# Kernel tuning notes

Measured on AMD Instinct MI355X. Metric: run time of the kernel, lower is better.

## Reference

```python
import jax, jax.numpy as jnp
import numpy as np


def setup_inputs() -> dict:
    key = jax.random.key(0)
    ks = jax.random.split(key, 6)
    B, T, H, U = 32, 2048, 1024, 1024
    return {
        "query": jax.random.normal(ks[0], (1, B, H), dtype=jnp.float32),
        "values": jax.random.normal(ks[1], (B, T, H), dtype=jnp.float32),
        "W_w": jax.random.normal(ks[2], (U, 2 * H), dtype=jnp.float32) * (1.0 / np.sqrt(2 * H)),
        "W_b": jax.random.normal(ks[3], (U,), dtype=jnp.float32) * 0.02,
        "V_w": jax.random.normal(ks[4], (1, U), dtype=jnp.float32) * (1.0 / np.sqrt(U)),
        "V_b": jax.random.normal(ks[5], (1,), dtype=jnp.float32) * 0.02,
    }


def reference(query, values, W_w, W_b, V_w, V_b):
    # query: [1, B, H] -> [B, H]; values: [B, T, H]
    q = query[0]  # squeeze dim 0
    H = values.shape[-1]
    # Split W over the concat dim instead of materializing cat([values, q_rep]):
    # cat @ W.T == values @ W[:, :H].T + q @ W[:, H:].T  (same math as torch)
    Wv, Wq = W_w[:, :H], W_w[:, H:]
    pre = (jnp.einsum("bth,uh->btu", values, Wv)
           + jnp.einsum("bh,uh->bu", q, Wq)[:, None, :]
           + W_b)  # [B, T, U]
    score = jnp.tanh(pre) @ V_w[0] + V_b[0]  # [B, T]
    attention_weights = jax.nn.softmax(score, axis=1)[..., None]  # [B, T, 1]
    context_vector = jnp.sum(attention_weights * values, axis=1)  # [B, H]
    return (context_vector, attention_weights)
```

## Files before the change

### kernel.cpp

```cpp
#include <hip/hip_runtime.h>
#include <hip/hip_bf16.h>


#define B_DIM 32
#define T_DIM 2048
#define H_DIM 1024
#define U_DIM 1024

typedef __bf16 bf16x8 __attribute__((ext_vector_type(8)));
typedef float f32x4 __attribute__((ext_vector_type(4)));

__device__ __forceinline__ unsigned int f2bf(float f) {
    unsigned int u = __float_as_uint(f);
    return (u + 0x7FFFu + ((u >> 16) & 1u)) >> 16;
}

__device__ __forceinline__ float fast_tanh(float x) {
    x = fminf(9.f, fmaxf(-9.f, x));
    float e = __expf(2.f * x);
    return 1.f - 2.f * __frcp_rn(e + 1.f);
}

__global__ void prep_wv_kernel(const float* __restrict__ W_w,
                               unsigned short* __restrict__ wv) {
    int u = blockIdx.x;
    int tid = threadIdx.x;
    float4 x = reinterpret_cast<const float4*>(W_w + (size_t)u * 2 * H_DIM)[tid];
    uint2 p;
    p.x = f2bf(x.x) | (f2bf(x.y) << 16);
    p.y = f2bf(x.z) | (f2bf(x.w) << 16);
    reinterpret_cast<uint2*>(wv)[(size_t)u * (H_DIM / 4) + tid] = p;
}

__global__ void prep_c_kernel(const float* __restrict__ q,
                              const float* __restrict__ W_w,
                              const float* __restrict__ W_b,
                              float* __restrict__ cvec) {
    __shared__ float4 q_sh[4][H_DIM / 4];
    int bg = blockIdx.y;
    int u0 = blockIdx.x * 64;
    int tid = threadIdx.x;
    int lane = tid & 63, w = tid >> 6;
#pragma unroll
    for (int i = 0; i < 4; i++)
        q_sh[i][tid] = reinterpret_cast<const float4*>(
            q + (size_t)(bg * 4 + i) * H_DIM)[tid];
    __syncthreads();
#pragma unroll
    for (int i = 0; i < 16; i++) {
        int u = u0 + w * 16 + i;
        const float4* wr = reinterpret_cast<const float4*>(W_w + (size_t)u * 2 * H_DIM + H_DIM);
        float s0 = 0.f, s1 = 0.f, s2 = 0.f, s3 = 0.f;
#pragma unroll
        for (int j = 0; j < 4; j++) {
            float4 wv4 = wr[j * 64 + lane];
            float4 qa = q_sh[0][j * 64 + lane];
            float4 qb = q_sh[1][j * 64 + lane];
            float4 qc = q_sh[2][j * 64 + lane];
            float4 qd = q_sh[3][j * 64 + lane];
            s0 += wv4.x * qa.x + wv4.y * qa.y + wv4.z * qa.z + wv4.w * qa.w;
            s1 += wv4.x * qb.x + wv4.y * qb.y + wv4.z * qb.z + wv4.w * qb.w;
            s2 += wv4.x * qc.x + wv4.y * qc.y + wv4.z * qc.z + wv4.w * qc.w;
            s3 += wv4.x * qd.x + wv4.y * qd.y + wv4.z * qd.z + wv4.w * qd.w;
        }
#pragma unroll
        for (int off = 32; off >= 1; off >>= 1) {
            s0 += __shfl_xor(s0, off, 64);
            s1 += __shfl_xor(s1, off, 64);
            s2 += __shfl_xor(s2, off, 64);
            s3 += __shfl_xor(s3, off, 64);
        }
        if (lane == 0) {
            float bb = W_b[u];
            cvec[(size_t)(bg * 4 + 0) * U_DIM + u] = s0 + bb;
            cvec[(size_t)(bg * 4 + 1) * U_DIM + u] = s1 + bb;
            cvec[(size_t)(bg * 4 + 2) * U_DIM + u] = s2 + bb;
            cvec[(size_t)(bg * 4 + 3) * U_DIM + u] = s3 + bb;
        }
    }
}

__global__ __launch_bounds__(512, 2)
void gemm_score_kernel(const float* __restrict__ values,
                       const unsigned short* __restrict__ wv,
                       const float* __restrict__ cvec,
                       const float* __restrict__ Vw,
                       float* __restrict__ score) {
    __shared__ __align__(16) unsigned short a_sh[2][64 * 72];
    __shared__ float sc_sh[64 * 8];

    const int tid = threadIdx.x;
    const int lane = tid & 63;
    const int w = tid >> 6;
    const int col = lane & 15;
    const int quad = lane >> 4;
    const int m0 = blockIdx.x * 64;
    const int b = m0 >> 11;
    const int t0 = m0 & (T_DIM - 1);

    f32x4 acc[4][8];
    const f32x4 zero4 = {0.f, 0.f, 0.f, 0.f};
#pragma unroll
    for (int mt = 0; mt < 4; mt++)
#pragma unroll
        for (int nt = 0; nt < 8; nt++) acc[mt][nt] = zero4;

    const int srow = tid >> 3;
    const int skg = tid & 7;
    const float* aptr = values + (size_t)(m0 + srow) * H_DIM + skg * 8;
    const int sidx = srow * 72 + skg * 8;

    {
        float4 n0 = reinterpret_cast<const float4*>(aptr)[0];
        float4 n1 = reinterpret_cast<const float4*>(aptr)[1];
        uint4 pk;
        pk.x = f2bf(n0.x) | (f2bf(n0.y) << 16);
        pk.y = f2bf(n0.z) | (f2bf(n0.w) << 16);
        pk.z = f2bf(n1.x) | (f2bf(n1.y) << 16);
        pk.w = f2bf(n1.z) | (f2bf(n1.w) << 16);
        *reinterpret_cast<uint4*>(&a_sh[0][sidx]) = pk;
    }
    __syncthreads();

    const unsigned short* bbase = wv + (size_t)(w * 128 + col) * H_DIM + quad * 8;

    for (int ks = 0; ks < 16; ks++) {
        const int cur = ks & 1;

        bf16x8 bf[2][8];
#pragma unroll
        for (int kk = 0; kk < 2; kk++)
#pragma unroll
            for (int nt = 0; nt < 8; nt++)
                bf[kk][nt] = *reinterpret_cast<const bf16x8*>(
                    bbase + (size_t)nt * 16 * H_DIM + ks * 64 + kk * 32);

        __builtin_amdgcn_sched_barrier(0x38F);

        float4 n0, n1;
        if (ks < 15) {
            const float* ap = aptr + (ks + 1) * 64;
            n0 = reinterpret_cast<const float4*>(ap)[0];
            n1 = reinterpret_cast<const float4*>(ap)[1];
        }
        __builtin_amdgcn_sched_barrier(0x387);

#pragma unroll
        for (int kk = 0; kk < 2; kk++) {
            bf16x8 af[4];
#pragma unroll
            for (int mt = 0; mt < 4; mt++)
                af[mt] = *reinterpret_cast<const bf16x8*>(
                    &a_sh[cur][(mt * 16 + col) * 72 + kk * 32 + quad * 8]);
#pragma unroll
            for (int nt = 0; nt < 8; nt++)
#pragma unroll
                for (int mt = 0; mt < 4; mt++)
                    acc[mt][nt] = __builtin_amdgcn_mfma_f32_16x16x32_bf16(
                        af[mt], bf[kk][nt], acc[mt][nt], 0, 0, 0);
        }

        if (ks < 15) {
            uint4 pk;
            pk.x = f2bf(n0.x) | (f2bf(n0.y) << 16);
            pk.y = f2bf(n0.z) | (f2bf(n0.w) << 16);
            pk.z = f2bf(n1.x) | (f2bf(n1.y) << 16);
            pk.w = f2bf(n1.z) | (f2bf(n1.w) << 16);
            *reinterpret_cast<uint4*>(&a_sh[1 - cur][sidx]) = pk;
        }
        __syncthreads();
    }

    float cv[8], vwv[8];
#pragma unroll
    for (int nt = 0; nt < 8; nt++) {
        int n = w * 128 + nt * 16 + col;
        cv[nt] = cvec[(size_t)b * U_DIM + n];
        vwv[nt] = Vw[n];
    }
#pragma unroll
    for (int mt = 0; mt < 4; mt++) {
#pragma unroll
        for (int j = 0; j < 4; j++) {
            float s = 0.f;
#pragma unroll
            for (int nt = 0; nt < 8; nt++)
                s += fast_tanh(acc[mt][nt][j] + cv[nt]) * vwv[nt];
            s += __shfl_xor(s, 1, 64);
            s += __shfl_xor(s, 2, 64);
            s += __shfl_xor(s, 4, 64);
            s += __shfl_xor(s, 8, 64);
            if (col == 0) sc_sh[(mt * 16 + quad * 4 + j) * 8 + w] = s;
        }
    }
    __syncthreads();
    if (tid < 64) {
        float s = 0.f;
#pragma unroll
        for (int ww = 0; ww < 8; ww++) s += sc_sh[tid * 8 + ww];
        score[(size_t)b * T_DIM + t0 + tid] = s;
    }
}

__global__ void softmax_kernel(const float* __restrict__ score,
                               float* __restrict__ aw) {
    int b = blockIdx.x;
    int tid = threadIdx.x;
    int lane = tid & 63, w = tid >> 6;
    __shared__ float redm[4];
    __shared__ float reds[4];
    float loc[8];
    float m = -1e30f;
#pragma unroll
    for (int i = 0; i < 8; i++) {
        loc[i] = score[(size_t)b * T_DIM + tid + i * 256];
        m = fmaxf(m, loc[i]);
    }
#pragma unroll
    for (int off = 32; off >= 1; off >>= 1) m = fmaxf(m, __shfl_xor(m, off, 64));
    if (lane == 0) redm[w] = m;
    __syncthreads();
    m = fmaxf(fmaxf(redm[0], redm[1]), fmaxf(redm[2], redm[3]));
    float sum = 0.f;
#pragma unroll
    for (int i = 0; i < 8; i++) {
        loc[i] = __expf(loc[i] - m);
        sum += loc[i];
    }
#pragma unroll
    for (int off = 32; off >= 1; off >>= 1) sum += __shfl_xor(sum, off, 64);
    if (lane == 0) reds[w] = sum;
    __syncthreads();
    sum = reds[0] + reds[1] + reds[2] + reds[3];
    float inv = 1.0f / sum;
#pragma unroll
    for (int i = 0; i < 8; i++)
        aw[(size_t)b * T_DIM + tid + i * 256] = loc[i] * inv;
}

__global__ void ctx_partial_kernel(const float* __restrict__ values,
                                   const float* __restrict__ aw,
                                   float* __restrict__ partial) {
    int tc = blockIdx.x;
    int b = blockIdx.y;
    int tid = threadIdx.x;
    const float4* v4 = reinterpret_cast<const float4*>(
                           values + ((size_t)b * T_DIM + tc * 128) * H_DIM) + tid;
    const float* a = aw + (size_t)b * T_DIM + tc * 128;
    float4 acc = make_float4(0.f, 0.f, 0.f, 0.f);
#pragma unroll 4
    for (int t = 0; t < 128; t++) {
        float wgt = a[t];
        float4 vv = v4[(size_t)t * (H_DIM / 4)];
        acc.x += wgt * vv.x; acc.y += wgt * vv.y;
        acc.z += wgt * vv.z; acc.w += wgt * vv.w;
    }
    reinterpret_cast<float4*>(partial + ((size_t)b * 16 + tc) * H_DIM)[tid] = acc;
}

__global__ void ctx_combine_kernel(const float* __restrict__ partial,
                                   float* __restrict__ ctx) {
    int idx = blockIdx.x * 256 + threadIdx.x;
    int b = idx >> 10, h = idx & (H_DIM - 1);
    float s = 0.f;
#pragma unroll
    for (int tc = 0; tc < 16; tc++)
        s += partial[((size_t)b * 16 + tc) * H_DIM + h];
    ctx[idx] = s;
}

extern "C" void kernel_launch(void* const* d_in, const int* in_sizes, int n_in,
                              void* d_out, int out_size, void* d_ws, size_t ws_size,
                              hipStream_t stream) {
    const float* query  = (const float*)d_in[0];
    const float* values = (const float*)d_in[1];
    const float* W_w    = (const float*)d_in[2];
    const float* W_b    = (const float*)d_in[3];
    const float* V_w    = (const float*)d_in[4];

    float* out = (float*)d_out;
    char* ws = (char*)d_ws;
    float* cvec            = (float*)(ws);
    unsigned short* wv     = (unsigned short*)(ws + 131072);
    float* score           = (float*)(ws + 131072 + 2097152);
    float* partial         = (float*)(ws + 131072 + 2097152 + 262144);
    float* ctx = out;
    float* aw  = out + B_DIM * H_DIM;

    prep_wv_kernel<<<U_DIM, 256, 0, stream>>>(W_w, wv);
    prep_c_kernel<<<dim3(U_DIM / 64, B_DIM / 4), 256, 0, stream>>>(query, W_w, W_b, cvec);
    gemm_score_kernel<<<(B_DIM * T_DIM) / 64, 512, 0, stream>>>(values, wv, cvec, V_w, score);
    softmax_kernel<<<B_DIM, 256, 0, stream>>>(score, aw);
    ctx_partial_kernel<<<dim3(16, B_DIM), 256, 0, stream>>>(values, aw, partial);
    ctx_combine_kernel<<<128, 256, 0, stream>>>(partial, ctx);
}
```

Measured before the change: 692.1 us.

## Retile score GEMM to 256x256 LDS-staged tiles and fuse softmax with context

The score GEMM moves from 64-row tiles that read W directly from global memory into registers to 256x256 output tiles. Both operands are staged through double-buffered, XOR-swizzled LDS, and blocks are ordered so that neighbours share tiles. Each N-tile writes a partial score, and the combined softmax-context kernel sums the four partials, recomputes the softmax in every block, and accumulates the context with atomics. The context output is zeroed in prep_c. This removes the redundant W traffic and two kernel launches, but adds recomputation of the softmax reduction per block, atomic contention, and a large LDS footprint that may lower occupancy.

```diff
diff --git a/kernel.cpp b/kernel.cpp
--- a/kernel.cpp
+++ b/kernel.cpp
@@ -35,12 +35,14 @@
 __global__ void prep_c_kernel(const float* __restrict__ q,
                               const float* __restrict__ W_w,
                               const float* __restrict__ W_b,
-                              float* __restrict__ cvec) {
+                              float* __restrict__ cvec,
+                              float* __restrict__ ctx) {
     __shared__ float4 q_sh[4][H_DIM / 4];
     int bg = blockIdx.y;
     int u0 = blockIdx.x * 64;
     int tid = threadIdx.x;
     int lane = tid & 63, w = tid >> 6;
+    ctx[(size_t)(blockIdx.y * 16 + blockIdx.x) * 256 + tid] = 0.f;
 #pragma unroll
     for (int i = 0; i < 4; i++)
         q_sh[i][tid] = reinterpret_cast<const float4*>(
@@ -85,136 +87,169 @@
                        const unsigned short* __restrict__ wv,
                        const float* __restrict__ cvec,
                        const float* __restrict__ Vw,
-                       float* __restrict__ score) {
-    __shared__ __align__(16) unsigned short a_sh[2][64 * 72];
-    __shared__ float sc_sh[64 * 8];
+                       float* __restrict__ score_part) {
+    __shared__ __align__(16) unsigned short a_sh[2][256 * 64];
+    __shared__ __align__(16) unsigned short b_sh[2][256 * 64];
 
     const int tid = threadIdx.x;
     const int lane = tid & 63;
     const int w = tid >> 6;
     const int col = lane & 15;
     const int quad = lane >> 4;
-    const int m0 = blockIdx.x * 64;
+    const int wr = w >> 2;
+    const int wc = w & 3;
+
+    const int work = (blockIdx.x & 7) * 128 + (blockIdx.x >> 3);
+    const int mtile = work >> 2;
+    const int ntile = work & 3;
+    const int m0 = mtile * 256;
     const int b = m0 >> 11;
-    const int t0 = m0 & (T_DIM - 1);
-
-    f32x4 acc[4][8];
+
+    f32x4 acc[8][4];
     const f32x4 zero4 = {0.f, 0.f, 0.f, 0.f};
 #pragma unroll
-    for (int mt = 0; mt < 4; mt++)
-#pragma unroll
-        for (int nt = 0; nt < 8; nt++) acc[mt][nt] = zero4;
-
-    const int srow = tid >> 3;
-    const int skg = tid & 7;
-    const float* aptr = values + (size_t)(m0 + srow) * H_DIM + skg * 8;
-    const int sidx = srow * 72 + skg * 8;
+    for (int mt = 0; mt < 8; mt++)
+#pragma unroll
+        for (int nt = 0; nt < 4; nt++) acc[mt][nt] = zero4;
+
+    const float4* v4 = reinterpret_cast<const float4*>(values);
+    const uint4* wv4 = reinterpret_cast<const uint4*>(wv);
+
+    const int arb = tid >> 4;
+    const int ak16 = tid & 15;
+    const int asw = (arb & 7) << 3;
+    const int bn = tid >> 1;
+    const int bkh = tid & 1;
+    const int bsw = (bn & 7) << 3;
 
     {
-        float4 n0 = reinterpret_cast<const float4*>(aptr)[0];
-        float4 n1 = reinterpret_cast<const float4*>(aptr)[1];
-        uint4 pk;
-        pk.x = f2bf(n0.x) | (f2bf(n0.y) << 16);
-        pk.y = f2bf(n0.z) | (f2bf(n0.w) << 16);
-        pk.z = f2bf(n1.x) | (f2bf(n1.y) << 16);
-        pk.w = f2bf(n1.z) | (f2bf(n1.w) << 16);
-        *reinterpret_cast<uint4*>(&a_sh[0][sidx]) = pk;
-    }
-    __syncthreads();
-
-    const unsigned short* bbase = wv + (size_t)(w * 128 + col) * H_DIM + quad * 8;
+        uint4 bstg[4];
+        const uint4* bgl = wv4 + (size_t)(ntile * 256 + bn) * 128 + bkh * 4;
+#pragma unroll
+        for (int j = 0; j < 4; j++) bstg[j] = bgl[j];
+        float4 astg[8];
+        const float4* agl = v4 + (size_t)(m0 + arb) * 256 + ak16;
+#pragma unroll
+        for (int j = 0; j < 8; j++) astg[j] = agl[(size_t)8192 * j];
+#pragma unroll
+        for (int j = 0; j < 4; j++)
+            *reinterpret_cast<uint4*>(&b_sh[0][bn * 64 + ((bkh * 32 + j * 8) ^ bsw)]) = bstg[j];
+#pragma unroll
+        for (int j = 0; j < 8; j++) {
+            uint2 p;
+            p.x = f2bf(astg[j].x) | (f2bf(astg[j].y) << 16);
+            p.y = f2bf(astg[j].z) | (f2bf(astg[j].w) << 16);
+            *reinterpret_cast<uint2*>(&a_sh[0][(arb + 32 * j) * 64 + ((ak16 * 4) ^ asw)]) = p;
+        }
+    }
+    __syncthreads();
+
+    const int swz = (col & 7) << 3;
 
     for (int ks = 0; ks < 16; ks++) {
         const int cur = ks & 1;
 
-        bf16x8 bf[2][8];
-#pragma unroll
-        for (int kk = 0; kk < 2; kk++)
-#pragma unroll
-            for (int nt = 0; nt < 8; nt++)
-                bf[kk][nt] = *reinterpret_cast<const bf16x8*>(
-                    bbase + (size_t)nt * 16 * H_DIM + ks * 64 + kk * 32);
-
+        uint4 bstg[4];
+        float4 astg[8];
+        if (ks < 15) {
+            const uint4* bgl = wv4 + (size_t)(ntile * 256 + bn) * 128 + (ks + 1) * 8 + bkh * 4;
+#pragma unroll
+            for (int j = 0; j < 4; j++) bstg[j] = bgl[j];
+            const float4* agl = v4 + (size_t)(m0 + arb) * 256 + (ks + 1) * 16 + ak16;
+#pragma unroll
+            for (int j = 0; j < 8; j++) astg[j] = agl[(size_t)8192 * j];
+        }
         __builtin_amdgcn_sched_barrier(0x38F);
 
-        float4 n0, n1;
+#pragma unroll
+        for (int kk = 0; kk < 2; kk++) {
+            bf16x8 af[8];
+            bf16x8 bf[4];
+#pragma unroll
+            for (int mt = 0; mt < 8; mt++)
+                af[mt] = *reinterpret_cast<const bf16x8*>(
+                    &a_sh[cur][(wr * 128 + mt * 16 + col) * 64 + ((kk * 32 + quad * 8) ^ swz)]);
+#pragma unroll
+            for (int nt = 0; nt < 4; nt++)
+                bf[nt] = *reinterpret_cast<const bf16x8*>(
+                    &b_sh[cur][(wc * 64 + nt * 16 + col) * 64 + ((kk * 32 + quad * 8) ^ swz)]);
+#pragma unroll
+            for (int nt = 0; nt < 4; nt++)
+#pragma unroll
+                for (int mt = 0; mt < 8; mt++)
+                    acc[mt][nt] = __builtin_amdgcn_mfma_f32_16x16x32_bf16(
+                        af[mt], bf[nt], acc[mt][nt], 0, 0, 0);
+            if (kk == 0 && ks < 15) {
+#pragma unroll
+                for (int j = 0; j < 4; j++)
+                    *reinterpret_cast<uint4*>(
+                        &b_sh[1 - cur][bn * 64 + ((bkh * 32 + j * 8) ^ bsw)]) = bstg[j];
+            }
+        }
+
         if (ks < 15) {
-            const float* ap = aptr + (ks + 1) * 64;
-            n0 = reinterpret_cast<const float4*>(ap)[0];
-            n1 = reinterpret_cast<const float4*>(ap)[1];
-        }
-        __builtin_amdgcn_sched_barrier(0x387);
-
-#pragma unroll
-        for (int kk = 0; kk < 2; kk++) {
-            bf16x8 af[4];
-#pragma unroll
-            for (int mt = 0; mt < 4; mt++)
-                af[mt] = *reinterpret_cast<const bf16x8*>(
-                    &a_sh[cur][(mt * 16 + col) * 72 + kk * 32 + quad * 8]);
-#pragma unroll
-            for (int nt = 0; nt < 8; nt++)
-#pragma unroll
-                for (int mt = 0; mt < 4; mt++)
-                    acc[mt][nt] = __builtin_amdgcn_mfma_f32_16x16x32_bf16(
-                        af[mt], bf[kk][nt], acc[mt][nt], 0, 0, 0);
-        }
-
-        if (ks < 15) {
-            uint4 pk;
-            pk.x = f2bf(n0.x) | (f2bf(n0.y) << 16);
-            pk.y = f2bf(n0.z) | (f2bf(n0.w) << 16);
-            pk.z = f2bf(n1.x) | (f2bf(n1.y) << 16);
-            pk.w = f2bf(n1.z) | (f2bf(n1.w) << 16);
-            *reinterpret_cast<uint4*>(&a_sh[1 - cur][sidx]) = pk;
+#pragma unroll
+            for (int j = 0; j < 8; j++) {
+                uint2 p;
+                p.x = f2bf(astg[j].x) | (f2bf(astg[j].y) << 16);
+                p.y = f2bf(astg[j].z) | (f2bf(astg[j].w) << 16);
+                *reinterpret_cast<uint2*>(
+                    &a_sh[1 - cur][(arb + 32 * j) * 64 + ((ak16 * 4) ^ asw)]) = p;
+            }
         }
         __syncthreads();
     }
 
-    float cv[8], vwv[8];
-#pragma unroll
-    for (int nt = 0; nt < 8; nt++) {
-        int n = w * 128 + nt * 16 + col;
+    float* sc = reinterpret_cast<float*>(a_sh);
+    float cv[4], vwv[4];
+#pragma unroll
+    for (int nt = 0; nt < 4; nt++) {
+        int n = ntile * 256 + wc * 64 + nt * 16 + col;
         cv[nt] = cvec[(size_t)b * U_DIM + n];
         vwv[nt] = Vw[n];
     }
 #pragma unroll
-    for (int mt = 0; mt < 4; mt++) {
+    for (int mt = 0; mt < 8; mt++) {
 #pragma unroll
         for (int j = 0; j < 4; j++) {
             float s = 0.f;
 #pragma unroll
-            for (int nt = 0; nt < 8; nt++)
+            for (int nt = 0; nt < 4; nt++)
                 s += fast_tanh(acc[mt][nt][j] + cv[nt]) * vwv[nt];
             s += __shfl_xor(s, 1, 64);
             s += __shfl_xor(s, 2, 64);
             s += __shfl_xor(s, 4, 64);
             s += __shfl_xor(s, 8, 64);
-            if (col == 0) sc_sh[(mt * 16 + quad * 4 + j) * 8 + w] = s;
-        }
-    }
-    __syncthreads();
-    if (tid < 64) {
-        float s = 0.f;
-#pragma unroll
-        for (int ww = 0; ww < 8; ww++) s += sc_sh[tid * 8 + ww];
-        score[(size_t)b * T_DIM + t0 + tid] = s;
-    }
-}
-
-__global__ void softmax_kernel(const float* __restrict__ score,
-                               float* __restrict__ aw) {
-    int b = blockIdx.x;
+            if (col == 0) sc[(wr * 128 + mt * 16 + quad * 4 + j) * 4 + wc] = s;
+        }
+    }
+    __syncthreads();
+    if (tid < 256) {
+        float s = sc[tid * 4] + sc[tid * 4 + 1] + sc[tid * 4 + 2] + sc[tid * 4 + 3];
+        score_part[(size_t)ntile * (B_DIM * T_DIM) + m0 + tid] = s;
+    }
+}
+
+__global__ void ctx_sm_kernel(const float* __restrict__ values,
+                              const float* __restrict__ score_part,
+                              float* __restrict__ aw,
+                              float* __restrict__ ctx) {
+    int tc = blockIdx.x;
+    int b = blockIdx.y;
     int tid = threadIdx.x;
     int lane = tid & 63, w = tid >> 6;
     __shared__ float redm[4];
     __shared__ float reds[4];
+    __shared__ float aw_sh[128];
+    const float* sp = score_part + (size_t)b * T_DIM;
     float loc[8];
     float m = -1e30f;
 #pragma unroll
     for (int i = 0; i < 8; i++) {
-        loc[i] = score[(size_t)b * T_DIM + tid + i * 256];
-        m = fmaxf(m, loc[i]);
+        int t = tid + i * 256;
+        float s = sp[t] + sp[65536 + t] + sp[131072 + t] + sp[196608 + t];
+        loc[i] = s;
+        m = fmaxf(m, s);
     }
 #pragma unroll
     for (int off = 32; off >= 1; off >>= 1) m = fmaxf(m, __shfl_xor(m, off, 64));
@@ -233,40 +268,29 @@
     __syncthreads();
     sum = reds[0] + reds[1] + reds[2] + reds[3];
     float inv = 1.0f / sum;
-#pragma unroll
-    for (int i = 0; i < 8; i++)
-        aw[(size_t)b * T_DIM + tid + i * 256] = loc[i] * inv;
-}
-
-__global__ void ctx_partial_kernel(const float* __restrict__ values,
-                                   const float* __restrict__ aw,
-                                   float* __restrict__ partial) {
-    int tc = blockIdx.x;
-    int b = blockIdx.y;
-    int tid = threadIdx.x;
+    if (tid < 128) {
+        int t = tc * 128 + tid;
+        float s = sp[t] + sp[65536 + t] + sp[131072 + t] + sp[196608 + t];
+        float av = __expf(s - m) * inv;
+        aw[(size_t)b * T_DIM + t] = av;
+        aw_sh[tid] = av;
+    }
+    __syncthreads();
     const float4* v4 = reinterpret_cast<const float4*>(
                            values + ((size_t)b * T_DIM + tc * 128) * H_DIM) + tid;
-    const float* a = aw + (size_t)b * T_DIM + tc * 128;
-    float4 acc = make_float4(0.f, 0.f, 0.f, 0.f);
+    float4 a = make_float4(0.f, 0.f, 0.f, 0.f);
 #pragma unroll 4
     for (int t = 0; t < 128; t++) {
-        float wgt = a[t];
+        float wgt = aw_sh[t];
         float4 vv = v4[(size_t)t * (H_DIM / 4)];
-        acc.x += wgt * vv.x; acc.y += wgt * vv.y;
-        acc.z += wgt * vv.z; acc.w += wgt * vv.w;
-    }
-    reinterpret_cast<float4*>(partial + ((size_t)b * 16 + tc) * H_DIM)[tid] = acc;
-}
-
-__global__ void ctx_combine_kernel(const float* __restrict__ partial,
-                                   float* __restrict__ ctx) {
-    int idx = blockIdx.x * 256 + threadIdx.x;
-    int b = idx >> 10, h = idx & (H_DIM - 1);
-    float s = 0.f;
-#pragma unroll
-    for (int tc = 0; tc < 16; tc++)
-        s += partial[((size_t)b * 16 + tc) * H_DIM + h];
-    ctx[idx] = s;
+        a.x += wgt * vv.x; a.y += wgt * vv.y;
+        a.z += wgt * vv.z; a.w += wgt * vv.w;
+    }
+    float* cp = ctx + (size_t)b * H_DIM + tid * 4;
+    atomicAdd(cp + 0, a.x);
+    atomicAdd(cp + 1, a.y);
+    atomicAdd(cp + 2, a.z);
+    atomicAdd(cp + 3, a.w);
 }
 
 extern "C" void kernel_launch(void* const* d_in, const int* in_sizes, int n_in,
@@ -282,15 +306,12 @@
     char* ws = (char*)d_ws;
     float* cvec            = (float*)(ws);
     unsigned short* wv     = (unsigned short*)(ws + 131072);
-    float* score           = (float*)(ws + 131072 + 2097152);
-    float* partial         = (float*)(ws + 131072 + 2097152 + 262144);
+    float* score_part      = (float*)(ws + 131072 + 2097152);
     float* ctx = out;
     float* aw  = out + B_DIM * H_DIM;
 
     prep_wv_kernel<<<U_DIM, 256, 0, stream>>>(W_w, wv);
-    prep_c_kernel<<<dim3(U_DIM / 64, B_DIM / 4), 256, 0, stream>>>(query, W_w, W_b, cvec);
-    gemm_score_kernel<<<(B_DIM * T_DIM) / 64, 512, 0, stream>>>(values, wv, cvec, V_w, score);
-    softmax_kernel<<<B_DIM, 256, 0, stream>>>(score, aw);
-    ctx_partial_kernel<<<dim3(16, B_DIM), 256, 0, stream>>>(values, aw, partial);
-    ctx_combine_kernel<<<128, 256, 0, stream>>>(partial, ctx);
-}
+    prep_c_kernel<<<dim3(U_DIM / 64, B_DIM / 4), 256, 0, stream>>>(query, W_w, W_b, cvec, ctx);
+    gemm_score_kernel<<<1024, 512, 0, stream>>>(values, wv, cvec, V_w, score_part);
+    ctx_sm_kernel<<<dim3(16, B_DIM), 256, 0, stream>>>(values, score_part, aw, ctx);
+}
```

After: 770.9 us. 1.11x slower.

## Split GEMM N into two tiles, register-prefetch B, hardware bf16 convert

Applied to the files above, without the earlier changes.

The score GEMM now runs 256-thread blocks that each cover 64 rows by 512 units, so the U dimension is split across two blocks. Each block writes a partial score that the softmax kernel adds back together. The K loop uses 32-wide steps with ping-pong register prefetch of the W fragments, v_cvt_pk_bf16_f32 for conversion, s_setprio around the MFMAs, and a remapped block order. The context reduction uses more chunks and stages the attention weights in LDS. The trade-offs are that values are read and converted twice and the K loop issues twice as many barriers.

```diff
diff --git a/kernel.cpp b/kernel.cpp
--- a/kernel.cpp
+++ b/kernel.cpp
@@ -13,6 +13,12 @@
 __device__ __forceinline__ unsigned int f2bf(float f) {
     unsigned int u = __float_as_uint(f);
     return (u + 0x7FFFu + ((u >> 16) & 1u)) >> 16;
+}
+
+__device__ __forceinline__ unsigned int cvt2(float lo, float hi) {
+    unsigned int r;
+    asm("v_cvt_pk_bf16_f32 %0, %1, %2" : "=v"(r) : "v"(lo), "v"(hi));
+    return r;
 }
 
 __device__ __forceinline__ float fast_tanh(float x) {
@@ -80,23 +86,26 @@
     }
 }
 
-__global__ __launch_bounds__(512, 2)
+__global__ __launch_bounds__(256, 2)
 void gemm_score_kernel(const float* __restrict__ values,
                        const unsigned short* __restrict__ wv,
                        const float* __restrict__ cvec,
                        const float* __restrict__ Vw,
-                       float* __restrict__ score) {
-    __shared__ __align__(16) unsigned short a_sh[2][64 * 72];
-    __shared__ float sc_sh[64 * 8];
+                       float* __restrict__ score_part) {
+    __shared__ __align__(16) unsigned short a_sh[2][64 * 32];
+    __shared__ float sc_sh[64 * 4];
 
     const int tid = threadIdx.x;
     const int lane = tid & 63;
     const int w = tid >> 6;
     const int col = lane & 15;
     const int quad = lane >> 4;
-    const int m0 = blockIdx.x * 64;
+
+    const int work = (blockIdx.x & 7) * 256 + (blockIdx.x >> 3);
+    const int mtile = work >> 1;
+    const int ntile = work & 1;
+    const int m0 = mtile * 64;
     const int b = m0 >> 11;
-    const int t0 = m0 & (T_DIM - 1);
 
     f32x4 acc[4][8];
     const f32x4 zero4 = {0.f, 0.f, 0.f, 0.f};
@@ -105,76 +114,71 @@
 #pragma unroll
         for (int nt = 0; nt < 8; nt++) acc[mt][nt] = zero4;
 
-    const int srow = tid >> 3;
-    const int skg = tid & 7;
-    const float* aptr = values + (size_t)(m0 + srow) * H_DIM + skg * 8;
-    const int sidx = srow * 72 + skg * 8;
-
+    const int arow = tid >> 2;
+    const int akq = tid & 3;
+    const float4* agl = reinterpret_cast<const float4*>(
+                            values + (size_t)(m0 + arow) * H_DIM) + akq * 2;
+    unsigned short* adst0 = &a_sh[0][arow * 32 + akq * 8];
+    unsigned short* adst1 = &a_sh[1][arow * 32 + akq * 8];
+
+    const char* bbase = (const char*)wv +
+        (size_t)(ntile * 512 + w * 128 + col) * 2048 + quad * 16;
+
+    bf16x8 bA[8], bB[8];
     {
-        float4 n0 = reinterpret_cast<const float4*>(aptr)[0];
-        float4 n1 = reinterpret_cast<const float4*>(aptr)[1];
+        float4 f0 = agl[0], f1 = agl[1];
         uint4 pk;
-        pk.x = f2bf(n0.x) | (f2bf(n0.y) << 16);
-        pk.y = f2bf(n0.z) | (f2bf(n0.w) << 16);
-        pk.z = f2bf(n1.x) | (f2bf(n1.y) << 16);
-        pk.w = f2bf(n1.z) | (f2bf(n1.w) << 16);
-        *reinterpret_cast<uint4*>(&a_sh[0][sidx]) = pk;
-    }
-    __syncthreads();
-
-    const unsigned short* bbase = wv + (size_t)(w * 128 + col) * H_DIM + quad * 8;
-
-    for (int ks = 0; ks < 16; ks++) {
-        const int cur = ks & 1;
-
-        bf16x8 bf[2][8];
-#pragma unroll
-        for (int kk = 0; kk < 2; kk++)
-#pragma unroll
-            for (int nt = 0; nt < 8; nt++)
-                bf[kk][nt] = *reinterpret_cast<const bf16x8*>(
-                    bbase + (size_t)nt * 16 * H_DIM + ks * 64 + kk * 32);
-
-        __builtin_amdgcn_sched_barrier(0x38F);
-
-        float4 n0, n1;
-        if (ks < 15) {
-            const float* ap = aptr + (ks + 1) * 64;
-            n0 = reinterpret_cast<const float4*>(ap)[0];
-            n1 = reinterpret_cast<const float4*>(ap)[1];
-        }
-        __builtin_amdgcn_sched_barrier(0x387);
-
-#pragma unroll
-        for (int kk = 0; kk < 2; kk++) {
-            bf16x8 af[4];
-#pragma unroll
-            for (int mt = 0; mt < 4; mt++)
-                af[mt] = *reinterpret_cast<const bf16x8*>(
-                    &a_sh[cur][(mt * 16 + col) * 72 + kk * 32 + quad * 8]);
-#pragma unroll
-            for (int nt = 0; nt < 8; nt++)
-#pragma unroll
-                for (int mt = 0; mt < 4; mt++)
-                    acc[mt][nt] = __builtin_amdgcn_mfma_f32_16x16x32_bf16(
-                        af[mt], bf[kk][nt], acc[mt][nt], 0, 0, 0);
-        }
-
-        if (ks < 15) {
-            uint4 pk;
-            pk.x = f2bf(n0.x) | (f2bf(n0.y) << 16);
-            pk.y = f2bf(n0.z) | (f2bf(n0.w) << 16);
-            pk.z = f2bf(n1.x) | (f2bf(n1.y) << 16);
-            pk.w = f2bf(n1.z) | (f2bf(n1.w) << 16);
-            *reinterpret_cast<uint4*>(&a_sh[1 - cur][sidx]) = pk;
-        }
-        __syncthreads();
-    }
+        pk.x = cvt2(f0.x, f0.y); pk.y = cvt2(f0.z, f0.w);
+        pk.z = cvt2(f1.x, f1.y); pk.w = cvt2(f1.z, f1.w);
+        *reinterpret_cast<uint4*>(adst0) = pk;
+#pragma unroll
+        for (int nt = 0; nt < 8; nt++)
+            bA[nt] = *reinterpret_cast<const bf16x8*>(bbase + (size_t)nt * 32768);
+    }
+    __syncthreads();
+
+#define GSTEP(CUR, KS, BC, BN) do {                                            \
+        float4 f0, f1;                                                         \
+        if ((KS) < 31) {                                                       \
+            f0 = agl[((KS) + 1) * 8];                                          \
+            f1 = agl[((KS) + 1) * 8 + 1];                                      \
+            _Pragma("unroll")                                                  \
+            for (int nt = 0; nt < 8; nt++)                                     \
+                BN[nt] = *reinterpret_cast<const bf16x8*>(                     \
+                    bbase + (size_t)nt * 32768 + ((KS) + 1) * 64);             \
+        }                                                                      \
+        bf16x8 af[4];                                                          \
+        _Pragma("unroll")                                                      \
+        for (int mt = 0; mt < 4; mt++)                                         \
+            af[mt] = *reinterpret_cast<const bf16x8*>(                         \
+                &a_sh[CUR][(mt * 16 + col) * 32 + quad * 8]);                  \
+        __builtin_amdgcn_s_setprio(1);                                         \
+        _Pragma("unroll")                                                      \
+        for (int nt = 0; nt < 8; nt++)                                         \
+            _Pragma("unroll")                                                  \
+            for (int mt = 0; mt < 4; mt++)                                     \
+                acc[mt][nt] = __builtin_amdgcn_mfma_f32_16x16x32_bf16(         \
+                    af[mt], BC[nt], acc[mt][nt], 0, 0, 0);                     \
+        __builtin_amdgcn_s_setprio(0);                                         \
+        if ((KS) < 31) {                                                       \
+            uint4 pk;                                                          \
+            pk.x = cvt2(f0.x, f0.y); pk.y = cvt2(f0.z, f0.w);                  \
+            pk.z = cvt2(f1.x, f1.y); pk.w = cvt2(f1.z, f1.w);                  \
+            *reinterpret_cast<uint4*>((CUR) ? adst0 : adst1) = pk;             \
+        }                                                                      \
+        __syncthreads();                                                       \
+    } while (0)
+
+    for (int k2 = 0; k2 < 16; k2++) {
+        GSTEP(0, 2 * k2, bA, bB);
+        GSTEP(1, 2 * k2 + 1, bB, bA);
+    }
+#undef GSTEP
 
     float cv[8], vwv[8];
 #pragma unroll
     for (int nt = 0; nt < 8; nt++) {
-        int n = w * 128 + nt * 16 + col;
+        int n = ntile * 512 + w * 128 + nt * 16 + col;
         cv[nt] = cvec[(size_t)b * U_DIM + n];
         vwv[nt] = Vw[n];
     }
@@ -190,30 +194,31 @@
             s += __shfl_xor(s, 2, 64);
             s += __shfl_xor(s, 4, 64);
             s += __shfl_xor(s, 8, 64);
-            if (col == 0) sc_sh[(mt * 16 + quad * 4 + j) * 8 + w] = s;
+            if (col == 0) sc_sh[(mt * 16 + quad * 4 + j) * 4 + w] = s;
         }
     }
     __syncthreads();
     if (tid < 64) {
-        float s = 0.f;
-#pragma unroll
-        for (int ww = 0; ww < 8; ww++) s += sc_sh[tid * 8 + ww];
-        score[(size_t)b * T_DIM + t0 + tid] = s;
-    }
-}
-
-__global__ void softmax_kernel(const float* __restrict__ score,
+        float s = sc_sh[tid * 4] + sc_sh[tid * 4 + 1] +
+                  sc_sh[tid * 4 + 2] + sc_sh[tid * 4 + 3];
+        score_part[(size_t)ntile * (B_DIM * T_DIM) + m0 + tid] = s;
+    }
+}
+
+__global__ void softmax_kernel(const float* __restrict__ score_part,
                                float* __restrict__ aw) {
     int b = blockIdx.x;
     int tid = threadIdx.x;
     int lane = tid & 63, w = tid >> 6;
     __shared__ float redm[4];
     __shared__ float reds[4];
+    const float* sp = score_part + (size_t)b * T_DIM;
     float loc[8];
     float m = -1e30f;
 #pragma unroll
     for (int i = 0; i < 8; i++) {
-        loc[i] = score[(size_t)b * T_DIM + tid + i * 256];
+        int t = tid + i * 256;
+        loc[i] = sp[t] + sp[B_DIM * T_DIM + t];
         m = fmaxf(m, loc[i]);
     }
 #pragma unroll
@@ -244,18 +249,20 @@
     int tc = blockIdx.x;
     int b = blockIdx.y;
     int tid = threadIdx.x;
+    __shared__ float aw_sh[64];
+    if (tid < 64) aw_sh[tid] = aw[(size_t)b * T_DIM + tc * 64 + tid];
+    __syncthreads();
     const float4* v4 = reinterpret_cast<const float4*>(
-                           values + ((size_t)b * T_DIM + tc * 128) * H_DIM) + tid;
-    const float* a = aw + (size_t)b * T_DIM + tc * 128;
-    float4 acc = make_float4(0.f, 0.f, 0.f, 0.f);
+                           values + ((size_t)b * T_DIM + tc * 64) * H_DIM) + tid;
+    float4 a = make_float4(0.f, 0.f, 0.f, 0.f);
 #pragma unroll 4
-    for (int t = 0; t < 128; t++) {
-        float wgt = a[t];
+    for (int t = 0; t < 64; t++) {
+        float wgt = aw_sh[t];
         float4 vv = v4[(size_t)t * (H_DIM / 4)];
-        acc.x += wgt * vv.x; acc.y += wgt * vv.y;
-        acc.z += wgt * vv.z; acc.w += wgt * vv.w;
-    }
-    reinterpret_cast<float4*>(partial + ((size_t)b * 16 + tc) * H_DIM)[tid] = acc;
+        a.x += wgt * vv.x; a.y += wgt * vv.y;
+        a.z += wgt * vv.z; a.w += wgt * vv.w;
+    }
+    reinterpret_cast<float4*>(partial + ((size_t)b * 32 + tc) * H_DIM)[tid] = a;
 }
 
 __global__ void ctx_combine_kernel(const float* __restrict__ partial,
@@ -264,8 +271,8 @@
     int b = idx >> 10, h = idx & (H_DIM - 1);
     float s = 0.f;
 #pragma unroll
-    for (int tc = 0; tc < 16; tc++)
-        s += partial[((size_t)b * 16 + tc) * H_DIM + h];
+    for (int tc = 0; tc < 32; tc++)
+        s += partial[((size_t)b * 32 + tc) * H_DIM + h];
     ctx[idx] = s;
 }
 
@@ -282,15 +289,15 @@
     char* ws = (char*)d_ws;
     float* cvec            = (float*)(ws);
     unsigned short* wv     = (unsigned short*)(ws + 131072);
-    float* score           = (float*)(ws + 131072 + 2097152);
-    float* partial         = (float*)(ws + 131072 + 2097152 + 262144);
+    float* score_part      = (float*)(ws + 131072 + 2097152);
+    float* partial         = (float*)(ws + 131072 + 2097152 + 524288);
     float* ctx = out;
     float* aw  = out + B_DIM * H_DIM;
 
     prep_wv_kernel<<<U_DIM, 256, 0, stream>>>(W_w, wv);
     prep_c_kernel<<<dim3(U_DIM / 64, B_DIM / 4), 256, 0, stream>>>(query, W_w, W_b, cvec);
-    gemm_score_kernel<<<(B_DIM * T_DIM) / 64, 512, 0, stream>>>(values, wv, cvec, V_w, score);
-    softmax_kernel<<<B_DIM, 256, 0, stream>>>(score, aw);
-    ctx_partial_kernel<<<dim3(16, B_DIM), 256, 0, stream>>>(values, aw, partial);
+    gemm_score_kernel<<<2048, 256, 0, stream>>>(values, wv, cvec, V_w, score_part);
+    softmax_kernel<<<B_DIM, 256, 0, stream>>>(score_part, aw);
+    ctx_partial_kernel<<<dim3(32, B_DIM), 256, 0, stream>>>(values, aw, partial);
     ctx_combine_kernel<<<128, 256, 0, stream>>>(partial, ctx);
 }
```

Measured after the change: 657.5 us. 5.0% less time.
